# Kernel optimization log

Measured on AMD Instinct MI355X. Metric: run time of the kernel, lower is better.

## Reference

```python
import jax, jax.numpy as jnp
import numpy as np

D_MODEL = 2048
N_HEADS = 16
HEAD_DIM = D_MODEL // N_HEADS  # 128
B, S, PAST = 2, 2048, 2048


def setup_inputs() -> dict:
    key = jax.random.key(0)
    ks = jax.random.split(key, 7)
    sc = 0.02
    return {
        "x": jax.random.normal(ks[0], (B, S, D_MODEL), dtype=jnp.float32),
        "past_k": jax.random.normal(ks[1], (B, N_HEADS, PAST, HEAD_DIM), dtype=jnp.float32),
        "past_v": jax.random.normal(ks[2], (B, N_HEADS, PAST, HEAD_DIM), dtype=jnp.float32),
        "Wq": jax.random.normal(ks[3], (D_MODEL, D_MODEL), dtype=jnp.float32) * sc,
        "Wk": jax.random.normal(ks[4], (D_MODEL, D_MODEL), dtype=jnp.float32) * sc,
        "Wv": jax.random.normal(ks[5], (D_MODEL, D_MODEL), dtype=jnp.float32) * sc,
        "Wo": jax.random.normal(ks[6], (D_MODEL, D_MODEL), dtype=jnp.float32) * sc,
    }


def reference(x, past_k, past_v, Wq, Wk, Wv, Wo):
    b, s, d = x.shape
    # nn.Linear(bias=False): y = x @ W.T ; split heads -> (B, H, S, hd)
    def proj_heads(W):
        return (x @ W.T).reshape(b, s, N_HEADS, HEAD_DIM).transpose(0, 2, 1, 3)
    q = proj_heads(Wq)
    k = proj_heads(Wk)
    v = proj_heads(Wv)
    # KV-cache append along sequence axis
    k = jnp.concatenate([past_k, k], axis=2)  # (B, H, full_S, hd)
    v = jnp.concatenate([past_v, v], axis=2)
    present = (k, v)
    full_s = k.shape[2]
    scores = jnp.einsum("bhqd,bhkd->bhqk", q, k) / (HEAD_DIM ** 0.5)
    # causal mask: query i (global pos past+i) may attend keys j <= past+i
    offset = full_s - s
    qi = jnp.arange(s)[:, None]
    kj = jnp.arange(full_s)[None, :]
    mask = kj > (qi + offset)  # triu with diagonal = full_s - s + 1
    scores = jnp.where(mask[None, None], -jnp.inf, scores)
    attn = jax.nn.softmax(scores, axis=-1)
    out = jnp.einsum("bhqk,bhkd->bhqd", attn, v)
    out = out.transpose(0, 2, 1, 3).reshape(b, s, d)
    output = out @ Wo.T
    return output, present
```

## Files before the change

kernel.cpp:

```cpp
#include <hip/hip_runtime.h>
#include <hip/hip_bf16.h>
#include <stdint.h>

typedef __attribute__((ext_vector_type(8))) short bf16x8;
typedef __attribute__((ext_vector_type(4))) float f32x4;
typedef __attribute__((ext_vector_type(16))) float f32x16;
typedef unsigned short u16;
typedef unsigned int u32;
typedef const __attribute__((address_space(1))) u32* gp_t;
typedef __attribute__((address_space(3))) u32* lp_t;

#define HD 128
#define NH 16
#define SEQ 2048
#define PASTN 2048
#define FULLS 4096
#define DM 2048

__device__ __forceinline__ u16 f2b(float f){
  union { float f; u32 u; } v; v.f = f;
  return (u16)((v.u + 0x7fffu + ((v.u >> 16) & 1u)) >> 16);
}
__device__ __forceinline__ float b2f(u16 b){
  union { u32 u; float f; } v; v.u = ((u32)b) << 16;
  return v.f;
}
__device__ __forceinline__ u32 cvtpk(float lo, float hi){
  u32 r; asm("v_cvt_pk_bf16_f32 %0, %1, %2" : "=v"(r) : "v"(lo), "v"(hi)); return r;
}
__device__ __forceinline__ f32x16 zero16(){ f32x16 z = {}; return z; }

__global__ void k_conv5(const float* __restrict__ sx,
                        const float* __restrict__ s1, const float* __restrict__ s2,
                        const float* __restrict__ s3, const float* __restrict__ s4,
                        u16* __restrict__ dx,
                        u16* __restrict__ d1, u16* __restrict__ d2,
                        u16* __restrict__ d3, u16* __restrict__ d4)
{
  const int total = 2097152 + 4 * 1048576;
  int i = blockIdx.x * blockDim.x + threadIdx.x;
  int stride = gridDim.x * blockDim.x;
  for (; i < total; i += stride){
    const float* s; u16* d; int off;
    if (i < 2097152){ s = sx; d = dx; off = i; }
    else {
      int t = i - 2097152;
      int seg = t >> 20; off = t & 1048575;
      s = (seg == 0) ? s1 : (seg == 1) ? s2 : (seg == 2) ? s3 : s4;
      d = (seg == 0) ? d1 : (seg == 1) ? d2 : (seg == 2) ? d3 : d4;
    }
    float4 v = ((const float4*)s)[off];
    ushort4 o = { f2b(v.x), f2b(v.y), f2b(v.z), f2b(v.w) };
    ((ushort4*)d)[off] = o;
  }
}

__global__ void k_past_k(const float* __restrict__ pk, float* __restrict__ outk,
                         u16* __restrict__ kb, int n4){
  int i = blockIdx.x * blockDim.x + threadIdx.x;
  int stride = gridDim.x * blockDim.x;
  for (; i < n4; i += stride){
    int g = i * 4;
    int c = g & 127;
    int r = g >> 7;
    int bh = r >> 11;
    int s = r & 2047;
    long dst = ((long)bh * FULLS + s) * HD + c;
    float4 v = ((const float4*)pk)[i];
    *(float4*)(outk + dst) = v;
    ushort4 o = { f2b(v.x), f2b(v.y), f2b(v.z), f2b(v.w) };
    *(ushort4*)(kb + dst) = o;
  }
}

__global__ void k_past_v(const float* __restrict__ pv, float* __restrict__ outv,
                         u16* __restrict__ vtb){
  __shared__ float tile[32][33];
  int bh = blockIdx.z;
  int d0 = blockIdx.x * 32;
  int s0 = blockIdx.y * 32;
  int tx = threadIdx.x, ty = threadIdx.y;
  const float* src = pv + (long)bh * PASTN * HD;
  float* dstv = outv + (long)bh * FULLS * HD;
#pragma unroll
  for (int k = 0; k < 4; k++){
    int si = ty + 8 * k;
    float v = src[(long)(s0 + si) * HD + d0 + tx];
    dstv[(long)(s0 + si) * HD + d0 + tx] = v;
    tile[si][tx] = v;
  }
  __syncthreads();
  u16* dstt = vtb + (long)bh * HD * FULLS;
#pragma unroll
  for (int k = 0; k < 4; k++){
    int di = ty + 8 * k;
    dstt[(long)(d0 + di) * FULLS + (s0 + tx)] = f2b(tile[tx][di]);
  }
}

__global__ __launch_bounds__(512, 1)
void k_gemm_qkv8(const u16* __restrict__ A,
                 const u16* __restrict__ Bq, const u16* __restrict__ Bk,
                 const u16* __restrict__ Bv,
                 u16* __restrict__ qb, u16* __restrict__ kbb,
                 u16* __restrict__ vtb,
                 float* __restrict__ outk, float* __restrict__ outv)
{
  __shared__ char LDS[131072];
  const int tid = threadIdx.x, w = tid >> 6, l = tid & 63;
  const int wm = w >> 2, wn = w & 3;
  const int m0 = blockIdx.y * 256;
  const int which = blockIdx.x >> 3;
  const u16* Bm = (which == 0) ? Bq : (which == 1) ? Bk : Bv;
  const int n0s = (blockIdx.x & 7) * 256;

  const int aoff0 = (((l >> 4) * 16) ^ ((l & 7) << 4));
  const int aoff1 = ((64 + (l >> 4) * 16) ^ ((l & 7) << 4));
  const char* ArdB = LDS + wm * 16384 + (l & 15) * 128;
  const char* BrdB = LDS + 65536 + (wn >> 1) * 16384 + (wn & 1) * 8192 + (l & 15) * 128;

  const int Pa = tid * 16, Pb = tid * 16 + 8192;
  const int ra = Pa >> 7, rb = Pb >> 7;
  const int sro1 = ra * 2048 + ((((Pa & 127) ^ ((ra & 7) << 4))) >> 1);
  const int sro2 = rb * 2048 + ((((Pb & 127) ^ ((rb & 7) << 4))) >> 1);
  char* sd1 = LDS + w * 1024;
  char* sd2 = LDS + w * 1024 + 8192;

  f32x4 acc[8][4] = {};

#define GLDS(SRC, DST) __builtin_amdgcn_global_load_lds((gp_t)(const void*)(SRC), (lp_t)(void*)(DST), 16, 0, 0)
#define STG(MAT, ROWB, C, REG) { const u16* s_ = (MAT) + (long)(ROWB) * 2048 + (C) * 64; \
    GLDS(s_ + sro1, sd1 + (REG)); GLDS(s_ + sro2, sd2 + (REG)); }
#define RDB(DST, PAR) { _Pragma("unroll") for (int nf = 0; nf < 4; nf++){ \
      DST[nf*2]   = *(const bf16x8*)(BrdB + (PAR)*32768 + nf*2048 + aoff0); \
      DST[nf*2+1] = *(const bf16x8*)(BrdB + (PAR)*32768 + nf*2048 + aoff1); } }
#define RDA(PAR, MF) \
      a0 = *(const bf16x8*)(ArdB + (PAR)*32768 + (MF)*2048 + aoff0); \
      a1 = *(const bf16x8*)(ArdB + (PAR)*32768 + (MF)*2048 + aoff1); \
      a2 = *(const bf16x8*)(ArdB + (PAR)*32768 + (MF+1)*2048 + aoff0); \
      a3 = *(const bf16x8*)(ArdB + (PAR)*32768 + (MF+1)*2048 + aoff1);
#define BARW { __builtin_amdgcn_s_barrier(); \
      asm volatile("s_waitcnt lgkmcnt(0)" ::: "memory"); \
      __builtin_amdgcn_sched_barrier(0); }
#define MM(BF, MF) { __builtin_amdgcn_s_setprio(1); \
      _Pragma("unroll") for (int nf = 0; nf < 4; nf++){ \
        acc[MF][nf]   = __builtin_amdgcn_mfma_f32_16x16x32_bf16(a0, BF[nf*2],   acc[MF][nf],   0,0,0); \
        acc[MF][nf]   = __builtin_amdgcn_mfma_f32_16x16x32_bf16(a1, BF[nf*2+1], acc[MF][nf],   0,0,0); \
        acc[MF+1][nf] = __builtin_amdgcn_mfma_f32_16x16x32_bf16(a2, BF[nf*2],   acc[MF+1][nf], 0,0,0); \
        acc[MF+1][nf] = __builtin_amdgcn_mfma_f32_16x16x32_bf16(a3, BF[nf*2+1], acc[MF+1][nf], 0,0,0); } \
      __builtin_amdgcn_s_setprio(0); }

  STG(A,  m0,        0, 0);
  STG(A,  m0 + 128,  0, 16384);
  STG(Bm, n0s,       0, 65536);
  STG(Bm, n0s + 128, 0, 81920);
  STG(Bm, n0s,       1, 98304);
  STG(Bm, n0s + 128, 1, 114688);
  asm volatile("s_waitcnt vmcnt(4)" ::: "memory");
  __builtin_amdgcn_s_barrier();

  for (int i = 0; i < 16; ++i){
    const int c1 = 2 * i + 1;
    const int cn = 2 * i + 2;
    const bool nlast = (i < 15);
    bf16x8 b0[8], b1[8];
    bf16x8 a0, a1, a2, a3;

    RDB(b0, 0); RDA(0, 0);
    STG(A, m0, c1, 32768);
    BARW; MM(b0, 0);
    __builtin_amdgcn_s_barrier();
    RDA(0, 2);
    STG(A, m0 + 128, c1, 49152);
    BARW; MM(b0, 2);
    __builtin_amdgcn_s_barrier();
    RDA(0, 4);
    if (nlast) STG(Bm, n0s, cn, 65536);
    BARW; MM(b0, 4);
    __builtin_amdgcn_s_barrier();
    RDA(0, 6);
    if (nlast) STG(Bm, n0s + 128, cn, 81920);
    BARW; MM(b0, 6);
    if (nlast) { asm volatile("s_waitcnt vmcnt(4)" ::: "memory"); }
    else       { asm volatile("s_waitcnt vmcnt(0)" ::: "memory"); }
    __builtin_amdgcn_s_barrier();
    RDB(b1, 1); RDA(1, 0);
    if (nlast) STG(A, m0, cn, 0);
    BARW; MM(b1, 0);
    __builtin_amdgcn_s_barrier();
    RDA(1, 2);
    if (nlast) STG(A, m0 + 128, cn, 16384);
    BARW; MM(b1, 2);
    __builtin_amdgcn_s_barrier();
    RDA(1, 4);
    if (nlast) STG(Bm, n0s, cn + 1, 98304);
    BARW; MM(b1, 4);
    __builtin_amdgcn_s_barrier();
    RDA(1, 6);
    if (nlast) STG(Bm, n0s + 128, cn + 1, 114688);
    BARW; MM(b1, 6);
    if (nlast) { asm volatile("s_waitcnt vmcnt(4)" ::: "memory"); }
    __builtin_amdgcn_s_barrier();
  }

#undef MM
#undef BARW
#undef RDA
#undef RDB
#undef STG
#undef GLDS

  const int rbase = m0 + wm * 128 + ((l >> 4) << 2);
  const int cb2 = n0s + wn * 64 + (l & 15);
#pragma unroll
  for (int mf = 0; mf < 8; mf++){
#pragma unroll
    for (int nf = 0; nf < 4; nf++){
      const int nl = cb2 + nf * 16;
      const int h = nl >> 7, dd = nl & 127;
      if (which == 2){
        const int mm = rbase + mf * 16;
        const int b = mm >> 11, s = mm & 2047;
        const int bh = b * NH + h;
        ushort4 pk = { f2b(acc[mf][nf][0]), f2b(acc[mf][nf][1]), f2b(acc[mf][nf][2]), f2b(acc[mf][nf][3]) };
        *(ushort4*)(vtb + ((long)bh * HD + dd) * FULLS + PASTN + s) = pk;
#pragma unroll
        for (int r = 0; r < 4; r++){
          long idx = ((long)bh * FULLS + PASTN + s + r) * HD + dd;
          outv[idx] = acc[mf][nf][r];
        }
      } else if (which == 1){
#pragma unroll
        for (int r = 0; r < 4; r++){
          const int mm = rbase + mf * 16 + r;
          const int b = mm >> 11, s = mm & 2047;
          long idx = (((long)(b * NH + h)) * FULLS + PASTN + s) * HD + dd;
          float v = acc[mf][nf][r];
          kbb[idx] = f2b(v);
          outk[idx] = v;
        }
      } else {
#pragma unroll
        for (int r = 0; r < 4; r++){
          const int mm = rbase + mf * 16 + r;
          const int b = mm >> 11, s = mm & 2047;
          qb[(((long)(b * NH + h)) * SEQ + s) * HD + dd] = f2b(acc[mf][nf][r]);
        }
      }
    }
  }
}

__global__ void k_gemm_o(const u16* __restrict__ A, const u16* __restrict__ Bm,
                         float* __restrict__ outf, int M, int N, int K)
{
  __shared__ u16 As[128 * 64];
  __shared__ u16 Bs[128 * 64];
  const int tid = threadIdx.x;
  const int w = tid >> 6, l = tid & 63;
  const int m0 = blockIdx.y * 128, n0 = blockIdx.x * 128;
  const int wr = w >> 1, wc = w & 1;
  const int lr = l & 15;
  const int lkb = (l >> 4) * 16;
  f32x4 acc[4][4] = {};

  for (int kt = 0; kt < K; kt += 64){
#pragma unroll
    for (int it = 0; it < 4; it++){
      int Pw = it * 4096 + w * 1024;
      int P = Pw + l * 16;
      int row = P >> 7, cb = P & 127;
      const u16* ga = A + (long)(m0 + row) * K + kt + (cb >> 1);
      __builtin_amdgcn_global_load_lds((gp_t)(const void*)ga, (lp_t)(void*)((char*)As + Pw), 16, 0, 0);
      const u16* gb = Bm + (long)(n0 + row) * K + kt + (cb >> 1);
      __builtin_amdgcn_global_load_lds((gp_t)(const void*)gb, (lp_t)(void*)((char*)Bs + Pw), 16, 0, 0);
    }
    __syncthreads();
#pragma unroll
    for (int kk = 0; kk < 2; kk++){
      bf16x8 af[4], bf[4];
#pragma unroll
      for (int i = 0; i < 4; i++){
        af[i] = *(const bf16x8*)((const char*)As + (wr * 64 + i * 16 + lr) * 128 + kk * 64 + lkb);
        bf[i] = *(const bf16x8*)((const char*)Bs + (wc * 64 + i * 16 + lr) * 128 + kk * 64 + lkb);
      }
#pragma unroll
      for (int i = 0; i < 4; i++)
#pragma unroll
        for (int j = 0; j < 4; j++)
          acc[i][j] = __builtin_amdgcn_mfma_f32_16x16x32_bf16(af[i], bf[j], acc[i][j], 0, 0, 0);
    }
    __syncthreads();
  }

  const int rbase = m0 + wr * 64 + ((l >> 4) << 2);
  const int cbase = n0 + wc * 64 + lr;
#pragma unroll
  for (int i = 0; i < 4; i++)
#pragma unroll
    for (int j = 0; j < 4; j++){
      const int nn = cbase + j * 16;
#pragma unroll
      for (int r = 0; r < 4; r++)
        outf[(long)(rbase + i * 16 + r) * N + nn] = acc[i][j][r];
    }
}

__global__ __launch_bounds__(256, 2)
void k_attn(const u16* __restrict__ qb, const u16* __restrict__ kb,
            const u16* __restrict__ vtb, u16* __restrict__ ab)
{
  __shared__ u16 Ks[2][64 * 128];
  __shared__ u16 Vs[2][128 * 64];
  const int tid = threadIdx.x, w = tid >> 6, l = tid & 63;
  const int lq = l & 31, hi = l >> 5;
  const int dd0 = blockIdx.x;
  const int xcd = dd0 & 7;
  const int j   = dd0 >> 3;
  const int ja = j >> 5, jb = (j >> 1) & 15, jc = j & 1;
  const int bh  = xcd * 4 + 2 * ja + jc;
  const int q0b = ((ja ^ jc) ? (15 - jb) : jb) << 7;
  const int qbase = q0b + w * 32;
  const int qpos = PASTN + qbase + lq;
  const u16* qhead = qb + (long)bh * SEQ * HD;
  const u16* khead = kb + (long)bh * FULLS * HD;
  const u16* vhead = vtb + (long)bh * HD * FULLS;

  const float qscale = 0.08838834764831845f * 1.4426950408889634f;
  bf16x8 qf[8];
#pragma unroll
  for (int ks = 0; ks < 8; ks++){
    bf16x8 tq = *(const bf16x8*)(qhead + (long)(qbase + lq) * HD + ks * 16 + hi * 8);
#pragma unroll
    for (int jj = 0; jj < 8; jj++) tq[jj] = (short)f2b(b2f((u16)tq[jj]) * qscale);
    qf[ks] = tq;
  }

  const int kswz = (lq & 15) << 4;
  const int vswz = (lq & 7) << 4;
  const char* kaddr[8];
#pragma unroll
  for (int ks = 0; ks < 8; ks++)
    kaddr[ks] = (const char*)Ks + lq * 256 + ((ks * 32 + hi * 16) ^ kswz);
  const char* vaddr[4];
#pragma unroll
  for (int ks2 = 0; ks2 < 4; ks2++)
    vaddr[ks2] = (const char*)Vs + lq * 128 + ((ks2 * 32 + hi * 16) ^ vswz);

  int ksrcoff[4], vsrcoff[4];
#pragma unroll
  for (int it = 0; it < 4; it++){
    int P = it * 4096 + w * 1024 + l * 16;
    ksrcoff[it] = P ^ (((P >> 8) & 15) << 4);
    int row = P >> 7;
    int cb = (P & 127) ^ ((row & 7) << 4);
    vsrcoff[it] = row * 8192 + cb;
  }

  auto stageK = [&](int t, int bufo){
    const char* src = (const char*)khead + ((long)t << 14);
    char* dstb = (char*)Ks + bufo + w * 1024;
#pragma unroll
    for (int it = 0; it < 4; it++)
      __builtin_amdgcn_global_load_lds((gp_t)(const void*)(src + ksrcoff[it]),
                                       (lp_t)(void*)(dstb + it * 4096), 16, 0, 0);
  };
  auto stageV = [&](int t, int bufo){
    const char* src = (const char*)vhead + ((long)t << 7);
    char* dstb = (char*)Vs + bufo + w * 1024;
#pragma unroll
    for (int it = 0; it < 4; it++)
      __builtin_amdgcn_global_load_lds((gp_t)(const void*)(src + vsrcoff[it]),
                                       (lp_t)(void*)(dstb + it * 4096), 16, 0, 0);
  };

  f32x16 acc[4] = {};
  float m_run = -1e30f, l_run = 0.f;
  const int ntiles = (PASTN + q0b + 128) >> 6;

  auto finishPV = [&](f32x16& sp0, f32x16& sp1, int vbufo){
    float a0[8];
#pragma unroll
    for (int i = 0; i < 8; i++)
      a0[i] = fmaxf(fmaxf(sp0[i], sp0[i + 8]), fmaxf(sp1[i], sp1[i + 8]));
    float mx = fmaxf(fmaxf(fmaxf(a0[0], a0[1]), fmaxf(a0[2], a0[3])),
                     fmaxf(fmaxf(a0[4], a0[5]), fmaxf(a0[6], a0[7])));
    { float xa = mx, xb = mx;
      asm("v_permlane32_swap_b32 %0, %1" : "+v"(xa), "+v"(xb));
      mx = fmaxf(xa, xb); }

    if (!__all(mx <= m_run + 8.f)){
      float mnew = fmaxf(m_run, mx);
      float corr = __builtin_exp2f(m_run - mnew);
      m_run = mnew; l_run *= corr;
#pragma unroll
      for (int r = 0; r < 16; r++){
        int qlr = (r & 3) + 8 * (r >> 2) + 4 * hi;
        float cr = __shfl(corr, qlr);
#pragma unroll
        for (int d2 = 0; d2 < 4; d2++) acc[d2][r] *= cr;
      }
    }

    float rs = 0.f;
#pragma unroll
    for (int r = 0; r < 16; r++){
      sp0[r] = __builtin_exp2f(sp0[r] - m_run); rs += sp0[r];
      sp1[r] = __builtin_exp2f(sp1[r] - m_run); rs += sp1[r];
    }
    { float ra = rs, rb = rs;
      asm("v_permlane32_swap_b32 %0, %1" : "+v"(ra), "+v"(rb));
      l_run += ra + rb; }

    bf16x8 pfrag[4];
#pragma unroll
    for (int kb2 = 0; kb2 < 2; kb2++){
      const f32x16& sp = kb2 ? sp1 : sp0;
#pragma unroll
      for (int half = 0; half < 2; half++){
        const int h8 = half * 8;
        u32 A0 = cvtpk(sp[h8 + 0], sp[h8 + 1]);
        u32 A1 = cvtpk(sp[h8 + 2], sp[h8 + 3]);
        u32 B0 = cvtpk(sp[h8 + 4], sp[h8 + 5]);
        u32 B1 = cvtpk(sp[h8 + 6], sp[h8 + 7]);
        asm("v_permlane32_swap_b32 %0, %1" : "+v"(A0), "+v"(B0));
        asm("v_permlane32_swap_b32 %0, %1" : "+v"(A1), "+v"(B1));
        union { u32 wd[4]; bf16x8 v; } F;
        F.wd[0] = A0; F.wd[1] = A1; F.wd[2] = B0; F.wd[3] = B1;
        pfrag[kb2 * 2 + half] = F.v;
      }
    }

    __builtin_amdgcn_s_setprio(1);
#pragma unroll
    for (int ks2 = 0; ks2 < 4; ks2++)
#pragma unroll
      for (int d2 = 0; d2 < 4; d2++){
        bf16x8 vf = *(const bf16x8*)(vaddr[ks2] + vbufo + d2 * 4096);
        acc[d2] = __builtin_amdgcn_mfma_f32_32x32x16_bf16(pfrag[ks2], vf, acc[d2], 0, 0, 0);
      }
    __builtin_amdgcn_s_setprio(0);
  };

#define QKT_MASK(T_, BUFC_, SC0_, SC1_)                                        \
  {                                                                            \
    SC0_ = zero16(); SC1_ = zero16();                                          \
    __builtin_amdgcn_s_setprio(1);                                             \
    _Pragma("unroll")                                                          \
    for (int ks = 0; ks < 8; ks++){                                            \
      bf16x8 kf0 = *(const bf16x8*)(kaddr[ks] + (BUFC_));                      \
      bf16x8 kf1 = *(const bf16x8*)(kaddr[ks] + (BUFC_) + 8192);               \
      SC0_ = __builtin_amdgcn_mfma_f32_32x32x16_bf16(kf0, qf[ks], SC0_, 0,0,0);\
      SC1_ = __builtin_amdgcn_mfma_f32_32x32x16_bf16(kf1, qf[ks], SC1_, 0,0,0);\
    }                                                                          \
    __builtin_amdgcn_s_setprio(0);                                             \
    const int kvb_ = (T_) * 64;                                                \
    if (kvb_ + 63 > PASTN + qbase){                                            \
      _Pragma("unroll")                                                        \
      for (int r = 0; r < 16; r++){                                            \
        int key = kvb_ + (r & 3) + 8 * (r >> 2) + 4 * hi;                      \
        if (key > qpos) SC0_[r] = -1e30f;                                      \
        if (key + 32 > qpos) SC1_[r] = -1e30f;                                 \
      }                                                                        \
    }                                                                          \
  }

#define STEP(T_, BUFC_, SP0_, SP1_, SC0_, SC1_)                                \
  {                                                                            \
    if ((T_) + 1 < ntiles) stageK((T_) + 1, (BUFC_) ^ 16384);                  \
    QKT_MASK(T_, BUFC_, SC0_, SC1_);                                           \
    finishPV(SP0_, SP1_, (BUFC_) ^ 16384);                                     \
    __syncthreads();                                                           \
    if ((T_) + 1 < ntiles) stageV((T_) + 1, (BUFC_) ^ 16384);                  \
  }

  f32x16 PA0, PA1, PB0, PB1;

  stageK(0, 0); stageV(0, 0);
  __syncthreads();

  stageK(1, 16384);
  QKT_MASK(0, 0, PA0, PA1);
  __syncthreads();
  stageV(1, 16384);

  for (int t = 1; t + 2 < ntiles; t += 2){
    STEP(t,     16384, PA0, PA1, PB0, PB1);
    STEP(t + 1, 0,     PB0, PB1, PA0, PA1);
  }
  STEP(ntiles - 1, 16384, PA0, PA1, PB0, PB1);
  finishPV(PB0, PB1, 16384);

#undef STEP
#undef QKT_MASK

  float inv = 1.0f / l_run;
  const int b = bh >> 4, h = bh & 15;
#pragma unroll
  for (int r = 0; r < 16; r++){
    int qlr = (r & 3) + 8 * (r >> 2) + 4 * hi;
    float ir = __shfl(inv, qlr);
    long rowbase = ((long)b * SEQ + (qbase + qlr)) * DM + h * HD;
#pragma unroll
    for (int d2 = 0; d2 < 4; d2++)
      ab[rowbase + d2 * 32 + lq] = f2b(acc[d2][r] * ir);
  }
}

extern "C" void kernel_launch(void* const* d_in, const int* in_sizes, int n_in,
                              void* d_out, int out_size, void* d_ws, size_t ws_size,
                              hipStream_t stream) {
  const float* x      = (const float*)d_in[0];
  const float* past_k = (const float*)d_in[1];
  const float* past_v = (const float*)d_in[2];
  const float* Wq     = (const float*)d_in[3];
  const float* Wk     = (const float*)d_in[4];
  const float* Wv     = (const float*)d_in[5];
  const float* Wo     = (const float*)d_in[6];

  float* out  = (float*)d_out;
  float* outk = out + 8388608;
  float* outv = out + 25165824;

  char* ws = (char*)d_ws;
  u16* wqb = (u16*)ws;
  u16* wkb = (u16*)(ws + 8388608);
  u16* wvb = (u16*)(ws + 16777216);
  u16* wob = (u16*)(ws + 25165824);
  u16* xb  = (u16*)(ws + 33554432);
  u16* qb  = (u16*)(ws + 50331648);
  u16* kb  = (u16*)(ws + 67108864);
  u16* vtb = (u16*)(ws + 100663296);
  u16* ab  = xb;

  k_conv5<<<2048, 256, 0, stream>>>(x, Wq, Wk, Wv, Wo, xb, wqb, wkb, wvb, wob);
  k_past_k<<<2048, 256, 0, stream>>>(past_k, outk, kb, 2097152);
  k_past_v<<<dim3(4, 64, 32), dim3(32, 8), 0, stream>>>(past_v, outv, vtb);

  k_gemm_qkv8<<<dim3(24, 16), 512, 0, stream>>>(xb, wqb, wkb, wvb,
                                                qb, kb, vtb, outk, outv);

  k_attn<<<512, 256, 0, stream>>>(qb, kb, vtb, ab);

  k_gemm_o<<<dim3(16, 32), 256, 0, stream>>>(ab, wob, out, 4096, 2048, 2048);
}
```

Baseline: 402.1 us.

## Fuse past-KV copy/convert kernels into QKV GEMM launch as extra blocks

Removes the separate past_k and past_v copy/convert/transpose kernels and runs that work in 128 extra blocks of the QKV GEMM launch, which now has 512 blocks (384 GEMM plus 128 copy). The memory-bound cache copy can then overlap with the compute-bound GEMM on CUs not busy with GEMM tiles, and two launches disappear. The copy blocks reserve the full 128KB LDS allocation and need 512 threads, and the GEMM grid mapping is flattened to 1D.

```diff
diff --git a/kernel.cpp b/kernel.cpp
--- a/kernel.cpp
+++ b/kernel.cpp
@@ -55,64 +55,75 @@
   }
 }
 
-__global__ void k_past_k(const float* __restrict__ pk, float* __restrict__ outk,
-                         u16* __restrict__ kb, int n4){
-  int i = blockIdx.x * blockDim.x + threadIdx.x;
-  int stride = gridDim.x * blockDim.x;
-  for (; i < n4; i += stride){
-    int g = i * 4;
-    int c = g & 127;
-    int r = g >> 7;
-    int bh = r >> 11;
-    int s = r & 2047;
-    long dst = ((long)bh * FULLS + s) * HD + c;
-    float4 v = ((const float4*)pk)[i];
-    *(float4*)(outk + dst) = v;
-    ushort4 o = { f2b(v.x), f2b(v.y), f2b(v.z), f2b(v.w) };
-    *(ushort4*)(kb + dst) = o;
-  }
-}
-
-__global__ void k_past_v(const float* __restrict__ pv, float* __restrict__ outv,
-                         u16* __restrict__ vtb){
-  __shared__ float tile[32][33];
-  int bh = blockIdx.z;
-  int d0 = blockIdx.x * 32;
-  int s0 = blockIdx.y * 32;
-  int tx = threadIdx.x, ty = threadIdx.y;
-  const float* src = pv + (long)bh * PASTN * HD;
-  float* dstv = outv + (long)bh * FULLS * HD;
-#pragma unroll
-  for (int k = 0; k < 4; k++){
-    int si = ty + 8 * k;
-    float v = src[(long)(s0 + si) * HD + d0 + tx];
-    dstv[(long)(s0 + si) * HD + d0 + tx] = v;
-    tile[si][tx] = v;
-  }
-  __syncthreads();
-  u16* dstt = vtb + (long)bh * HD * FULLS;
-#pragma unroll
-  for (int k = 0; k < 4; k++){
-    int di = ty + 8 * k;
-    dstt[(long)(d0 + di) * FULLS + (s0 + tx)] = f2b(tile[tx][di]);
-  }
-}
-
 __global__ __launch_bounds__(512, 1)
-void k_gemm_qkv8(const u16* __restrict__ A,
+void k_qkv_fused(const u16* __restrict__ A,
                  const u16* __restrict__ Bq, const u16* __restrict__ Bk,
                  const u16* __restrict__ Bv,
                  u16* __restrict__ qb, u16* __restrict__ kbb,
                  u16* __restrict__ vtb,
-                 float* __restrict__ outk, float* __restrict__ outv)
+                 float* __restrict__ outk, float* __restrict__ outv,
+                 const float* __restrict__ pk, const float* __restrict__ pv)
 {
   __shared__ char LDS[131072];
-  const int tid = threadIdx.x, w = tid >> 6, l = tid & 63;
+  const int bx = blockIdx.x;
+  const int tid = threadIdx.x;
+
+  if (bx >= 384){
+    if (bx < 448){
+      for (int i = (bx - 384) * 512 + tid; i < 2097152; i += 32768){
+        int g = i * 4;
+        int c = g & 127;
+        int r = g >> 7;
+        int bh = r >> 11;
+        int s = r & 2047;
+        long dst = ((long)bh * FULLS + s) * HD + c;
+        float4 v = ((const float4*)pk)[i];
+        *(float4*)(outk + dst) = v;
+        ushort4 o = { f2b(v.x), f2b(v.y), f2b(v.z), f2b(v.w) };
+        *(ushort4*)(kbb + dst) = o;
+      }
+    } else {
+      float* ldsF = (float*)LDS;
+      for (int cc = 0; cc < 16; cc++){
+        int c = ((bx - 448) << 4) + cc;
+        int bh = c >> 5, s0 = (c & 31) << 6;
+        const float* src = pv + ((long)bh * PASTN + s0) * HD;
+        float* dsv = outv + ((long)bh * FULLS + s0) * HD;
+#pragma unroll
+        for (int p = 0; p < 4; p++){
+          int idx = tid + p * 512;
+          int row = idx >> 5, c4 = (idx & 31) << 2;
+          float4 v = *(const float4*)(src + row * HD + c4);
+          *(float4*)(dsv + row * HD + c4) = v;
+          ldsF[row * 129 + c4 + 0] = v.x;
+          ldsF[row * 129 + c4 + 1] = v.y;
+          ldsF[row * 129 + c4 + 2] = v.z;
+          ldsF[row * 129 + c4 + 3] = v.w;
+        }
+        __syncthreads();
+        int d = tid >> 2, sb = (tid & 3) << 4;
+        u16* dst = vtb + ((long)bh * HD + d) * FULLS + s0 + sb;
+#pragma unroll
+        for (int g = 0; g < 4; g++){
+          ushort4 o = { f2b(ldsF[(sb + g * 4 + 0) * 129 + d]),
+                        f2b(ldsF[(sb + g * 4 + 1) * 129 + d]),
+                        f2b(ldsF[(sb + g * 4 + 2) * 129 + d]),
+                        f2b(ldsF[(sb + g * 4 + 3) * 129 + d]) };
+          *(ushort4*)(dst + g * 4) = o;
+        }
+        __syncthreads();
+      }
+    }
+    return;
+  }
+
+  const int w = tid >> 6, l = tid & 63;
   const int wm = w >> 2, wn = w & 3;
-  const int m0 = blockIdx.y * 256;
-  const int which = blockIdx.x >> 3;
+  const int which = bx >> 7;
+  const int r0 = bx & 127;
+  const int m0 = (r0 & 15) * 256;
+  const int n0s = (r0 >> 4) * 256;
   const u16* Bm = (which == 0) ? Bq : (which == 1) ? Bk : Bv;
-  const int n0s = (blockIdx.x & 7) * 256;
 
   const int aoff0 = (((l >> 4) * 16) ^ ((l & 7) << 4));
   const int aoff1 = ((64 + (l >> 4) * 16) ^ ((l & 7) << 4));
@@ -170,32 +181,39 @@
     STG(A, m0, c1, 32768);
     BARW; MM(b0, 0);
     __builtin_amdgcn_s_barrier();
+
     RDA(0, 2);
     STG(A, m0 + 128, c1, 49152);
     BARW; MM(b0, 2);
     __builtin_amdgcn_s_barrier();
+
     RDA(0, 4);
     if (nlast) STG(Bm, n0s, cn, 65536);
     BARW; MM(b0, 4);
     __builtin_amdgcn_s_barrier();
+
     RDA(0, 6);
     if (nlast) STG(Bm, n0s + 128, cn, 81920);
     BARW; MM(b0, 6);
     if (nlast) { asm volatile("s_waitcnt vmcnt(4)" ::: "memory"); }
     else       { asm volatile("s_waitcnt vmcnt(0)" ::: "memory"); }
     __builtin_amdgcn_s_barrier();
+
     RDB(b1, 1); RDA(1, 0);
     if (nlast) STG(A, m0, cn, 0);
     BARW; MM(b1, 0);
     __builtin_amdgcn_s_barrier();
+
     RDA(1, 2);
     if (nlast) STG(A, m0 + 128, cn, 16384);
     BARW; MM(b1, 2);
     __builtin_amdgcn_s_barrier();
+
     RDA(1, 4);
     if (nlast) STG(Bm, n0s, cn + 1, 98304);
     BARW; MM(b1, 4);
     __builtin_amdgcn_s_barrier();
+
     RDA(1, 6);
     if (nlast) STG(Bm, n0s + 128, cn + 1, 114688);
     BARW; MM(b1, 6);
@@ -222,8 +240,8 @@
         const int mm = rbase + mf * 16;
         const int b = mm >> 11, s = mm & 2047;
         const int bh = b * NH + h;
-        ushort4 pk = { f2b(acc[mf][nf][0]), f2b(acc[mf][nf][1]), f2b(acc[mf][nf][2]), f2b(acc[mf][nf][3]) };
-        *(ushort4*)(vtb + ((long)bh * HD + dd) * FULLS + PASTN + s) = pk;
+        ushort4 pkv = { f2b(acc[mf][nf][0]), f2b(acc[mf][nf][1]), f2b(acc[mf][nf][2]), f2b(acc[mf][nf][3]) };
+        *(ushort4*)(vtb + ((long)bh * HD + dd) * FULLS + PASTN + s) = pkv;
 #pragma unroll
         for (int r = 0; r < 4; r++){
           long idx = ((long)bh * FULLS + PASTN + s + r) * HD + dd;
@@ -534,11 +552,10 @@
   u16* ab  = xb;
 
   k_conv5<<<2048, 256, 0, stream>>>(x, Wq, Wk, Wv, Wo, xb, wqb, wkb, wvb, wob);
-  k_past_k<<<2048, 256, 0, stream>>>(past_k, outk, kb, 2097152);
-  k_past_v<<<dim3(4, 64, 32), dim3(32, 8), 0, stream>>>(past_v, outv, vtb);
-
-  k_gemm_qkv8<<<dim3(24, 16), 512, 0, stream>>>(xb, wqb, wkb, wvb,
-                                                qb, kb, vtb, outk, outv);
+
+  k_qkv_fused<<<512, 512, 0, stream>>>(xb, wqb, wkb, wvb,
+                                       qb, kb, vtb, outk, outv,
+                                       past_k, past_v);
 
   k_attn<<<512, 256, 0, stream>>>(qb, kb, vtb, ab);
 
```

Result: faster. 370.0 us (-8.0%).
